# Kernel optimization log

Hardware: AMD Instinct MI355X
Metric: run time of the kernel (lower is better)

## Reference

```python
import jax, jax.numpy as jnp
import numpy as np

DIM = 768
HEADS = 12
SCALE = DIM ** -0.5  # NOTE: module scales by full dim, not head dim


def setup_inputs() -> dict:
    key = jax.random.key(0)
    ks = jax.random.split(key, 5)
    B, N, C = 8, 1024, DIM
    x = jax.random.normal(ks[0], (B, N, C), dtype=jnp.float32)
    W_qkv = jax.random.normal(ks[1], (C, 3 * C), dtype=jnp.float32) * (C ** -0.5)
    b_qkv = jnp.zeros((3 * C,), dtype=jnp.float32)
    W_out = jax.random.normal(ks[2], (C, C), dtype=jnp.float32) * (C ** -0.5)
    b_out = jnp.zeros((C,), dtype=jnp.float32)
    return {"x": x, "W_qkv": W_qkv, "b_qkv": b_qkv, "W_out": W_out, "b_out": b_out}


def reference(x, W_qkv, b_qkv, W_out, b_out) -> jnp.ndarray:
    B, N, C = x.shape
    H, D = HEADS, C // HEADS
    qkv = x @ W_qkv + b_qkv                       # [B, N, 3C]
    q, k, v = jnp.split(qkv, 3, axis=-1)
    # [B, N, C] -> [B, H, N, D]
    q = q.reshape(B, N, H, D).transpose(0, 2, 1, 3)
    k = k.reshape(B, N, H, D).transpose(0, 2, 1, 3)
    v = v.reshape(B, N, H, D).transpose(0, 2, 1, 3)
    attn = jnp.einsum("bhnd,bhmd->bhnm", q, k) * SCALE
    attn = jax.nn.softmax(attn, axis=-1)
    out = jnp.einsum("bhnm,bhmd->bhnd", attn, v)   # [B, H, N, D]
    out = out.transpose(0, 2, 1, 3).reshape(B, N, C)
    return out @ W_out + b_out
```

## Files before the change

kernel.cpp:

```cpp
#include <hip/hip_runtime.h>
#include <hip/hip_bf16.h>

typedef __attribute__((ext_vector_type(4))) float f32x4;
typedef __attribute__((ext_vector_type(8))) short bf16x8;

#define SCALE_F 0.03608439182435161f
#define QSCALE  (0.03608439182435161f * 1.44269504088896f)

__device__ __forceinline__ unsigned short f2bf(float f) {
    union { float f; unsigned u; } v; v.f = f;
    return (unsigned short)((v.u + 0x7FFFu + ((v.u >> 16) & 1u)) >> 16);
}

__device__ __forceinline__ float fast_exp2(float x) {
#if __has_builtin(__builtin_amdgcn_exp2f)
    return __builtin_amdgcn_exp2f(x);
#else
    return exp2f(x);
#endif
}

__device__ __forceinline__ void gload_lds16(const void* g, void* l) {
    __builtin_amdgcn_global_load_lds(
        (const __attribute__((address_space(1))) unsigned int*)g,
        (__attribute__((address_space(3))) unsigned int*)l, 16, 0, 0);
}

__global__ __launch_bounds__(256) void xcvt_kernel(const float* __restrict__ X,
                                                   unsigned short* __restrict__ Xb,
                                                   int n8) {
    const int i = blockIdx.x * 256 + threadIdx.x;
    if (i < n8) {
        f32x4 a = *(const f32x4*)(X + (size_t)i * 8);
        f32x4 b = *(const f32x4*)(X + (size_t)i * 8 + 4);
        bf16x8 w;
#pragma unroll
        for (int j = 0; j < 4; ++j) { w[j] = (short)f2bf(a[j]); w[4 + j] = (short)f2bf(b[j]); }
        *(bf16x8*)(Xb + (size_t)i * 8) = w;
    }
}

__global__ __launch_bounds__(256) void wtrans_kernel(const float* __restrict__ W,
                                                     unsigned short* __restrict__ WT,
                                                     int R, int C) {
    __shared__ unsigned short T[64][68];
    const int t = threadIdx.x;
    const int r0 = blockIdx.y * 64, c0 = blockIdx.x * 64;
    {
        const int lr = t >> 4, lc = (t & 15) * 4;
#pragma unroll
        for (int p = 0; p < 4; ++p) {
            const float* s = W + (size_t)(r0 + lr + p * 16) * C + c0 + lc;
            f32x4 v = *(const f32x4*)s;
            unsigned short* d = &T[lr + p * 16][lc];
            d[0] = f2bf(v[0]); d[1] = f2bf(v[1]); d[2] = f2bf(v[2]); d[3] = f2bf(v[3]);
        }
    }
    __syncthreads();
    {
        const int oc = t >> 3, j0 = (t & 7) * 8;
#pragma unroll
        for (int p = 0; p < 2; ++p) {
            const int c = oc + p * 32;
            bf16x8 v;
#pragma unroll
            for (int j = 0; j < 8; ++j) v[j] = (short)T[j0 + j][c];
            *(bf16x8*)(WT + (size_t)(c0 + c) * R + r0 + j0) = v;
        }
    }
}

__global__ __launch_bounds__(256) void qkv_gemm_kernel(
    const unsigned short* __restrict__ Xb, const unsigned short* __restrict__ WT,
    const float* __restrict__ bias,
    unsigned short* __restrict__ Qw, unsigned short* __restrict__ Kw,
    unsigned short* __restrict__ VTw)
{
    __shared__ unsigned short Alds[128 * 32];
    __shared__ unsigned short Blds[128 * 32];

    const int t = threadIdx.x;
    const int lane = t & 63, wave = t >> 6;
    const int l15 = lane & 15, l4 = lane >> 4;
    const int m0 = blockIdx.x * 128, n0 = blockIdx.y * 128;
    const int wr = wave >> 1, wc = wave & 1;

    f32x4 acc[4][4];
#pragma unroll
    for (int m = 0; m < 4; ++m)
#pragma unroll
        for (int n = 0; n < 4; ++n) acc[m][n] = (f32x4){0.f, 0.f, 0.f, 0.f};

    for (int k0 = 0; k0 < 768; k0 += 32) {
#pragma unroll
        for (int c = 0; c < 2; ++c) {
            const int o = wave * 1024 + lane * 16 + c * 4096;
            const int row = o >> 6, cb = o & 63;
            gload_lds16((const char*)(Xb + (size_t)(m0 + row) * 768 + k0) + cb,
                        (char*)Alds + wave * 1024 + c * 4096);
            gload_lds16((const char*)(WT + (size_t)(n0 + row) * 768 + k0) + cb,
                        (char*)Blds + wave * 1024 + c * 4096);
        }
        __syncthreads();
        bf16x8 af[4], bfr[4];
#pragma unroll
        for (int m = 0; m < 4; ++m)
            af[m] = *(const bf16x8*)((const char*)Alds + (wr * 64 + m * 16 + l15) * 64 + l4 * 16);
#pragma unroll
        for (int n = 0; n < 4; ++n)
            bfr[n] = *(const bf16x8*)((const char*)Blds + (wc * 64 + n * 16 + l15) * 64 + l4 * 16);
#pragma unroll
        for (int m = 0; m < 4; ++m)
#pragma unroll
            for (int n = 0; n < 4; ++n)
                acc[m][n] = __builtin_amdgcn_mfma_f32_16x16x32_bf16(af[m], bfr[n], acc[m][n], 0, 0, 0);
        __syncthreads();
    }

#pragma unroll
    for (int n = 0; n < 4; ++n) {
        const int col = n0 + wc * 64 + n * 16 + l15;
        const float bv = bias[col];
        const int which = col / 768;
        const int cc = col - which * 768;
        const int h = cc >> 6, dd = cc & 63;
#pragma unroll
        for (int m = 0; m < 4; ++m) {
#pragma unroll
            for (int r = 0; r < 4; ++r) {
                const int row = m0 + wr * 64 + m * 16 + l4 * 4 + r;
                const int b = row >> 10, ntok = row & 1023;
                const size_t bh = (size_t)b * 12 + h;
                float val = acc[m][n][r] + bv;
                if (which == 0) val *= QSCALE;
                const unsigned short hv = f2bf(val);
                if (which == 0)      Qw[(bh * 1024 + ntok) * 64 + dd] = hv;
                else if (which == 1) Kw[(bh * 1024 + ntok) * 64 + dd] = hv;
                else                 VTw[(bh * 64 + dd) * 1024 + ntok] = hv;
            }
        }
    }
}

__global__ __launch_bounds__(256) void attn_kernel(
    const unsigned short* __restrict__ Qw, const unsigned short* __restrict__ Kw,
    const unsigned short* __restrict__ VTw, unsigned short* __restrict__ A2)
{
    __shared__ unsigned short Klds[2 * 64 * 64];
    __shared__ unsigned short Vlds[2 * 64 * 64];
    __shared__ unsigned short Plds[4 * 16 * 72];
    __shared__ float Flds[4 * 16];

    const int t = threadIdx.x, lane = t & 63, wave = t >> 6;
    const int l15 = lane & 15, l4 = lane >> 4;
    const int wg = (blockIdx.x & 7) * 192 + (blockIdx.x >> 3);
    const int qt = wg & 15, bh = wg >> 4;
    const int q0 = qt * 64;

    const size_t kvbase = (size_t)bh * 1024 * 64;
    const size_t vtbase = (size_t)bh * 64 * 1024;

    const unsigned short* qptr = Qw + kvbase + (size_t)(q0 + wave * 16 + l15) * 64;
    const bf16x8 qf0 = *(const bf16x8*)((const char*)qptr + l4 * 16);
    const bf16x8 qf1 = *(const bf16x8*)((const char*)qptr + 64 + l4 * 16);

    f32x4 oacc[4];
#pragma unroll
    for (int d = 0; d < 4; ++d) oacc[d] = (f32x4){0.f, 0.f, 0.f, 0.f};
    float m_run = -1e30f, l_run = 0.f;

    unsigned short* prow = &Plds[(wave * 16 + l15) * 72];

    auto STAGE = [&](int kt, int bufi) {
        const int kv0 = kt * 64;
        char* kb = (char*)Klds + bufi * 8192;
        char* vb = (char*)Vlds + bufi * 8192;
#pragma unroll
        for (int c = 0; c < 2; ++c) {
            const int oo = wave * 1024 + lane * 16 + c * 4096;
            const int row = oo >> 7, w = oo & 127;
            const int sw = w ^ ((row & 7) << 4);
            gload_lds16((const char*)(Kw + kvbase + (size_t)(kv0 + row) * 64) + sw,
                        kb + wave * 1024 + c * 4096);
            gload_lds16((const char*)(VTw + vtbase + (size_t)row * 1024 + kv0) + sw,
                        vb + wave * 1024 + c * 4096);
        }
    };

    STAGE(0, 0);
    for (int kt = 0; kt < 16; ++kt) {
        const int cur = kt & 1;
        if (kt < 15) {
            STAGE(kt + 1, cur ^ 1);
            asm volatile("s_waitcnt vmcnt(4)" ::: "memory");
        } else {
            asm volatile("s_waitcnt vmcnt(0)" ::: "memory");
        }
        __builtin_amdgcn_s_barrier();
        __builtin_amdgcn_sched_barrier(0);
        const char* kb = (const char*)Klds + cur * 8192;
        const char* vb = (const char*)Vlds + cur * 8192;

        f32x4 sacc[4];
#pragma unroll
        for (int i = 0; i < 4; ++i) sacc[i] = (f32x4){0.f, 0.f, 0.f, 0.f};
#pragma unroll
        for (int ks = 0; ks < 2; ++ks) {
            const bf16x8 qq = ks ? qf1 : qf0;
#pragma unroll
            for (int kvf = 0; kvf < 4; ++kvf) {
                const int row = kvf * 16 + l15;
                int addr = row * 128 + ks * 64 + l4 * 16;
                addr ^= (row & 7) << 4;
                const bf16x8 kf = *(const bf16x8*)(kb + addr);
                sacc[kvf] = __builtin_amdgcn_mfma_f32_16x16x32_bf16(kf, qq, sacc[kvf], 0, 0, 0);
            }
        }

        float p[16];
        float tmax = -1e30f;
#pragma unroll
        for (int i = 0; i < 4; ++i)
#pragma unroll
            for (int r = 0; r < 4; ++r) {
                p[i * 4 + r] = sacc[i][r];
                tmax = fmaxf(tmax, sacc[i][r]);
            }
        tmax = fmaxf(tmax, __shfl_xor(tmax, 16));
        tmax = fmaxf(tmax, __shfl_xor(tmax, 32));

        if (!__all(tmax - m_run <= 8.f)) {
            const float mnew = fmaxf(m_run, tmax);
            const float alpha = fast_exp2(m_run - mnew);
            m_run = mnew;
            if (lane < 16) Flds[wave * 16 + lane] = alpha;
            const f32x4 av = *(const f32x4*)(&Flds[wave * 16 + l4 * 4]);
#pragma unroll
            for (int d = 0; d < 4; ++d)
#pragma unroll
                for (int r = 0; r < 4; ++r) oacc[d][r] *= av[r];
            l_run *= alpha;
        }

        float tsum = 0.f;
#pragma unroll
        for (int i = 0; i < 16; ++i) { p[i] = fast_exp2(p[i] - m_run); tsum += p[i]; }
        tsum += __shfl_xor(tsum, 16);
        tsum += __shfl_xor(tsum, 32);
        l_run += tsum;

#pragma unroll
        for (int i = 0; i < 4; ++i) {
            unsigned lo, hi;
            asm("v_cvt_pk_bf16_f32 %0, %1, %2" : "=v"(lo) : "v"(p[i * 4 + 0]), "v"(p[i * 4 + 1]));
            asm("v_cvt_pk_bf16_f32 %0, %1, %2" : "=v"(hi) : "v"(p[i * 4 + 2]), "v"(p[i * 4 + 3]));
            const int kv = i * 16 + l4 * 4;
            *(unsigned*)(prow + kv) = lo;
            *(unsigned*)(prow + kv + 2) = hi;
        }

#pragma unroll
        for (int ks = 0; ks < 2; ++ks) {
            const bf16x8 pf = *(const bf16x8*)((const char*)prow + ks * 64 + l4 * 16);
#pragma unroll
            for (int df = 0; df < 4; ++df) {
                const int d = df * 16 + l15;
                int addr = d * 128 + ks * 64 + l4 * 16;
                addr ^= (d & 7) << 4;
                const bf16x8 vf = *(const bf16x8*)(vb + addr);
                oacc[df] = __builtin_amdgcn_mfma_f32_16x16x32_bf16(pf, vf, oacc[df], 0, 0, 0);
            }
        }
        __builtin_amdgcn_s_barrier();
    }

    if (lane < 16) Flds[wave * 16 + lane] = 1.f / l_run;
    __builtin_amdgcn_s_barrier();
    const f32x4 inv = *(const f32x4*)(&Flds[wave * 16 + l4 * 4]);
    const int b = bh / 12, h = bh - b * 12;
#pragma unroll
    for (int df = 0; df < 4; ++df) {
#pragma unroll
        for (int r = 0; r < 4; ++r) {
            const int row = b * 1024 + q0 + wave * 16 + l4 * 4 + r;
            const int col = h * 64 + df * 16 + l15;
            A2[(size_t)row * 768 + col] = f2bf(oacc[df][r] * inv[r]);
        }
    }
}

__global__ __launch_bounds__(256) void out_gemm_kernel(
    const unsigned short* __restrict__ A2, const unsigned short* __restrict__ WT,
    const float* __restrict__ bias, float* __restrict__ Out)
{
    __shared__ unsigned short Alds[128 * 32];
    __shared__ unsigned short Blds[128 * 32];

    const int t = threadIdx.x;
    const int lane = t & 63, wave = t >> 6;
    const int l15 = lane & 15, l4 = lane >> 4;
    const int m0 = blockIdx.x * 128, n0 = blockIdx.y * 128;
    const int wr = wave >> 1, wc = wave & 1;

    f32x4 acc[4][4];
#pragma unroll
    for (int m = 0; m < 4; ++m)
#pragma unroll
        for (int n = 0; n < 4; ++n) acc[m][n] = (f32x4){0.f, 0.f, 0.f, 0.f};

    for (int k0 = 0; k0 < 768; k0 += 32) {
#pragma unroll
        for (int c = 0; c < 2; ++c) {
            const int o = wave * 1024 + lane * 16 + c * 4096;
            const int row = o >> 6, cb = o & 63;
            gload_lds16((const char*)(A2 + (size_t)(m0 + row) * 768 + k0) + cb,
                        (char*)Alds + wave * 1024 + c * 4096);
            gload_lds16((const char*)(WT + (size_t)(n0 + row) * 768 + k0) + cb,
                        (char*)Blds + wave * 1024 + c * 4096);
        }
        __syncthreads();
        bf16x8 af[4], bfr[4];
#pragma unroll
        for (int m = 0; m < 4; ++m)
            af[m] = *(const bf16x8*)((const char*)Alds + (wr * 64 + m * 16 + l15) * 64 + l4 * 16);
#pragma unroll
        for (int n = 0; n < 4; ++n)
            bfr[n] = *(const bf16x8*)((const char*)Blds + (wc * 64 + n * 16 + l15) * 64 + l4 * 16);
#pragma unroll
        for (int m = 0; m < 4; ++m)
#pragma unroll
            for (int n = 0; n < 4; ++n)
                acc[m][n] = __builtin_amdgcn_mfma_f32_16x16x32_bf16(af[m], bfr[n], acc[m][n], 0, 0, 0);
        __syncthreads();
    }

#pragma unroll
    for (int n = 0; n < 4; ++n) {
        const int col = n0 + wc * 64 + n * 16 + l15;
        const float bv = bias[col];
#pragma unroll
        for (int m = 0; m < 4; ++m)
#pragma unroll
            for (int r = 0; r < 4; ++r) {
                const int row = m0 + wr * 64 + m * 16 + l4 * 4 + r;
                Out[(size_t)row * 768 + col] = acc[m][n][r] + bv;
            }
    }
}

extern "C" void kernel_launch(void* const* d_in, const int* in_sizes, int n_in,
                              void* d_out, int out_size, void* d_ws, size_t ws_size,
                              hipStream_t stream) {
    const float* X    = (const float*)d_in[0];
    const float* Wqkv = (const float*)d_in[1];
    const float* bqkv = (const float*)d_in[2];
    const float* Wout = (const float*)d_in[3];
    const float* bout = (const float*)d_in[4];
    float* Out = (float*)d_out;

    const size_t nq = (size_t)96 * 1024 * 64;
    unsigned short* XbA2  = (unsigned short*)d_ws;
    unsigned short* Qw    = XbA2 + nq;
    unsigned short* Kw    = Qw + nq;
    unsigned short* VTw   = Kw + nq;
    unsigned short* WqkvT = VTw + nq;
    unsigned short* WoutT = WqkvT + (size_t)2304 * 768;

    hipLaunchKernelGGL(xcvt_kernel, dim3(3072), dim3(256), 0, stream,
                       X, XbA2, 8192 * 768 / 8);
    hipLaunchKernelGGL(wtrans_kernel, dim3(36, 12), dim3(256), 0, stream,
                       Wqkv, WqkvT, 768, 2304);
    hipLaunchKernelGGL(wtrans_kernel, dim3(12, 12), dim3(256), 0, stream,
                       Wout, WoutT, 768, 768);
    hipLaunchKernelGGL(qkv_gemm_kernel, dim3(64, 18), dim3(256), 0, stream,
                       XbA2, WqkvT, bqkv, Qw, Kw, VTw);
    hipLaunchKernelGGL(attn_kernel, dim3(1536), dim3(256), 0, stream,
                       Qw, Kw, VTw, XbA2);
    hipLaunchKernelGGL(out_gemm_kernel, dim3(64, 6), dim3(256), 0, stream,
                       XbA2, WoutT, bout, Out);
}
```

Before: 143.0 us.

## Keep P in registers by permuting K rows, drop P LDS round-trip

Permutes the row order in which K tiles are staged into LDS so that each lane's S accumulator values line up with the bf16 A-operand layout needed by the PV MFMA. P can then be packed straight from registers instead of being written to and read back from a shared-memory scratch buffer. It also raises wave priority around the MFMA blocks with s_setprio and drops the final barrier before the normalization read. The removed barrier only guards an intra-wave Flds write/read, and the key-order permutation must stay consistent with V's column order, so correctness depends on the bit-shuffle being exact.

New measurement: 138.8 us. 3.0% less time.

```diff
diff --git a/kernel.cpp b/kernel.cpp
--- a/kernel.cpp
+++ b/kernel.cpp
@@ -2,6 +2,7 @@
 #include <hip/hip_bf16.h>
 
 typedef __attribute__((ext_vector_type(4))) float f32x4;
+typedef __attribute__((ext_vector_type(4))) unsigned u32x4;
 typedef __attribute__((ext_vector_type(8))) short bf16x8;
 
 #define SCALE_F 0.03608439182435161f
@@ -148,7 +149,6 @@
 {
     __shared__ unsigned short Klds[2 * 64 * 64];
     __shared__ unsigned short Vlds[2 * 64 * 64];
-    __shared__ unsigned short Plds[4 * 16 * 72];
     __shared__ float Flds[4 * 16];
 
     const int t = threadIdx.x, lane = t & 63, wave = t >> 6;
@@ -169,8 +169,6 @@
     for (int d = 0; d < 4; ++d) oacc[d] = (f32x4){0.f, 0.f, 0.f, 0.f};
     float m_run = -1e30f, l_run = 0.f;
 
-    unsigned short* prow = &Plds[(wave * 16 + l15) * 72];
-
     auto STAGE = [&](int kt, int bufi) {
         const int kv0 = kt * 64;
         char* kb = (char*)Klds + bufi * 8192;
@@ -178,11 +176,12 @@
 #pragma unroll
         for (int c = 0; c < 2; ++c) {
             const int oo = wave * 1024 + lane * 16 + c * 4096;
-            const int row = oo >> 7, w = oo & 127;
-            const int sw = w ^ ((row & 7) << 4);
-            gload_lds16((const char*)(Kw + kvbase + (size_t)(kv0 + row) * 64) + sw,
+            const int R = oo >> 7, w = oo & 127;
+            const int sw = w ^ ((R & 7) << 4);
+            const int kvs = (R & 0x23) | ((R & 0x0C) << 1) | ((R & 0x10) >> 2);
+            gload_lds16((const char*)(Kw + kvbase + (size_t)(kv0 + kvs) * 64) + sw,
                         kb + wave * 1024 + c * 4096);
-            gload_lds16((const char*)(VTw + vtbase + (size_t)row * 1024 + kv0) + sw,
+            gload_lds16((const char*)(VTw + vtbase + (size_t)R * 1024 + kv0) + sw,
                         vb + wave * 1024 + c * 4096);
         }
     };
@@ -204,6 +203,7 @@
         f32x4 sacc[4];
 #pragma unroll
         for (int i = 0; i < 4; ++i) sacc[i] = (f32x4){0.f, 0.f, 0.f, 0.f};
+        __builtin_amdgcn_s_setprio(1);
 #pragma unroll
         for (int ks = 0; ks < 2; ++ks) {
             const bf16x8 qq = ks ? qf1 : qf0;
@@ -216,6 +216,7 @@
                 sacc[kvf] = __builtin_amdgcn_mfma_f32_16x16x32_bf16(kf, qq, sacc[kvf], 0, 0, 0);
             }
         }
+        __builtin_amdgcn_s_setprio(0);
 
         float p[16];
         float tmax = -1e30f;
@@ -249,33 +250,34 @@
         tsum += __shfl_xor(tsum, 32);
         l_run += tsum;
 
-#pragma unroll
-        for (int i = 0; i < 4; ++i) {
-            unsigned lo, hi;
-            asm("v_cvt_pk_bf16_f32 %0, %1, %2" : "=v"(lo) : "v"(p[i * 4 + 0]), "v"(p[i * 4 + 1]));
-            asm("v_cvt_pk_bf16_f32 %0, %1, %2" : "=v"(hi) : "v"(p[i * 4 + 2]), "v"(p[i * 4 + 3]));
-            const int kv = i * 16 + l4 * 4;
-            *(unsigned*)(prow + kv) = lo;
-            *(unsigned*)(prow + kv + 2) = hi;
-        }
-
+        bf16x8 paf[2];
 #pragma unroll
         for (int ks = 0; ks < 2; ++ks) {
-            const bf16x8 pf = *(const bf16x8*)((const char*)prow + ks * 64 + l4 * 16);
+            union { u32x4 u; bf16x8 h; } cv;
+#pragma unroll
+            for (int j2 = 0; j2 < 4; ++j2)
+                asm("v_cvt_pk_bf16_f32 %0, %1, %2"
+                    : "=v"(cv.u[j2]) : "v"(p[ks * 8 + 2 * j2]), "v"(p[ks * 8 + 2 * j2 + 1]));
+            paf[ks] = cv.h;
+        }
+
+        __builtin_amdgcn_s_setprio(1);
+#pragma unroll
+        for (int ks = 0; ks < 2; ++ks) {
 #pragma unroll
             for (int df = 0; df < 4; ++df) {
                 const int d = df * 16 + l15;
                 int addr = d * 128 + ks * 64 + l4 * 16;
                 addr ^= (d & 7) << 4;
                 const bf16x8 vf = *(const bf16x8*)(vb + addr);
-                oacc[df] = __builtin_amdgcn_mfma_f32_16x16x32_bf16(pf, vf, oacc[df], 0, 0, 0);
-            }
-        }
+                oacc[df] = __builtin_amdgcn_mfma_f32_16x16x32_bf16(paf[ks], vf, oacc[df], 0, 0, 0);
+            }
+        }
+        __builtin_amdgcn_s_setprio(0);
         __builtin_amdgcn_s_barrier();
     }
 
     if (lane < 16) Flds[wave * 16 + lane] = 1.f / l_run;
-    __builtin_amdgcn_s_barrier();
     const f32x4 inv = *(const f32x4*)(&Flds[wave * 16 + l4 * 4]);
     const int b = bh / 12, h = bh - b * 12;
 #pragma unroll
```
